# Kernel tuning notes

Hardware: AMD Instinct MI355X
Metric: run time of the kernel (lower is better)

## Reference

```python
import jax, jax.numpy as jnp
import numpy as np

N = 50000
E = 800000
IN_DIM = 128
OUT_DIM = 128


def setup_inputs() -> dict:
    key = jax.random.key(0)
    k1, k2, k3, k4 = jax.random.split(key, 4)
    x = jax.random.normal(k1, (N, IN_DIM), dtype=jnp.float32)
    edge_index = jax.random.randint(k2, (2, E), 0, N, dtype=jnp.int64)
    # Linear(in_dim*2, out_dim) params
    W = jax.random.normal(k3, (2 * IN_DIM, OUT_DIM), dtype=jnp.float32) * (1.0 / np.sqrt(2 * IN_DIM))
    b = jax.random.normal(k4, (OUT_DIM,), dtype=jnp.float32) * 0.01
    return {"x": x, "edge_index": edge_index, "W": W, "b": b}


def reference(x, edge_index, W, b):
    src, dst = edge_index[0], edge_index[1]
    diff = x[src] - x[dst]                              # (E, C)
    # segment-max over destination nodes; empty segments get -inf identity
    seg_max = jax.ops.segment_max(diff, dst, num_segments=N)  # (N, C)
    counts = jax.ops.segment_sum(jnp.ones((E,), dtype=jnp.int32), dst, num_segments=N)
    # original code leaves zeros for nodes with no incoming edges
    max_diff = jnp.where((counts > 0)[:, None], seg_max, jnp.zeros_like(seg_max))
    x_cat = jnp.concatenate([x, max_diff], axis=-1)     # (N, 2C)
    return x_cat @ W + b
```

## Files before the change

### kernel.cpp

```cpp
#include <hip/hip_runtime.h>
#include <math.h>

#define NN 50000
#define NE 800000
#define CD 128
#define LINKB 1600

typedef __attribute__((ext_vector_type(8))) short short8;
typedef __attribute__((ext_vector_type(4))) float f32x4;


__device__ inline unsigned pack2bf(float lo, float hi) {
    unsigned a = __float_as_uint(lo), b = __float_as_uint(hi);
    a = (a + 0x7fffu + ((a >> 16) & 1u)) >> 16;
    b = (b + 0x7fffu + ((b >> 16) & 1u)) & 0xffff0000u;
    return a | b;
}

__device__ inline unsigned short f2bf(float f) {
    unsigned u = __float_as_uint(f);
    return (unsigned short)((u + 0x7fffu + ((u >> 16) & 1u)) >> 16);
}

__device__ inline void fmax8(float* m, uint4 v) {
    m[0] = fmaxf(m[0], __uint_as_float(v.x << 16));
    m[1] = fmaxf(m[1], __uint_as_float(v.x & 0xffff0000u));
    m[2] = fmaxf(m[2], __uint_as_float(v.y << 16));
    m[3] = fmaxf(m[3], __uint_as_float(v.y & 0xffff0000u));
    m[4] = fmaxf(m[4], __uint_as_float(v.z << 16));
    m[5] = fmaxf(m[5], __uint_as_float(v.z & 0xffff0000u));
    m[6] = fmaxf(m[6], __uint_as_float(v.w << 16));
    m[7] = fmaxf(m[7], __uint_as_float(v.w & 0xffff0000u));
}


__global__ __launch_bounds__(256) void prep2_k(const int* __restrict__ ei,
                                               const float* __restrict__ x,
                                               const float* __restrict__ W,
                                               int* __restrict__ head,
                                               int* __restrict__ next,
                                               unsigned* __restrict__ xb,
                                               unsigned short* __restrict__ wt) {
    int b = blockIdx.x;
    int t = threadIdx.x;
    if (b < LINKB) {
        for (int e = b * 256 + t; e < NE; e += LINKB * 256) {
            int d = ei[NE + e];
            int old = atomicExch(&head[d], e);
            next[e] = old;
        }
    } else {
        int tid = (b - LINKB) * 256 + t;
        if (tid < NN * CD / 4) {
            float4 v = ((const float4*)x)[tid];
            uint2 r;
            r.x = pack2bf(v.x, v.y);
            r.y = pack2bf(v.z, v.w);
            ((uint2*)xb)[tid] = r;
        } else {
            int i = tid - NN * CD / 4;
            if (i < 2 * CD * CD) {
                int n = i >> 8, k = i & 255;
                wt[(size_t)n * 256 + k] = f2bf(W[(size_t)k * 128 + n]);
            }
        }
    }
}


__global__ __launch_bounds__(256) void fused_k(const unsigned* __restrict__ xb,
                                               const int* __restrict__ head,
                                               const int* __restrict__ next,
                                               const int* __restrict__ srcp,
                                               const short* __restrict__ wt,
                                               const float* __restrict__ bias,
                                               float* __restrict__ out) {
    __shared__ unsigned short idx[64][68];
    __shared__ int ovf[64];
    __shared__ unsigned short amx[64][136];

    int t = threadIdx.x;
    int nbase = blockIdx.x * 64;

    if (t < 64) {
        int node = nbase + t;
        int e = (node < NN) ? head[node] : -1;
        int cnt = 0;
        while (e >= 0 && cnt < 64) {
            idx[t][cnt] = (unsigned short)srcp[e];
            e = next[e];
            cnt++;
        }
        idx[t][64] = (unsigned short)cnt;
        ovf[t] = e;
    }
    __syncthreads();

    int w = t >> 6, lane = t & 63;
    int q = lane >> 4, c = lane & 15;
#pragma unroll 1
    for (int j = 0; j < 4; j++) {
        int ln = w * 16 + j * 4 + q;
        int node = nbase + ln;
        int cnt = idx[ln][64];
        float m[8];
#pragma unroll
        for (int i = 0; i < 8; i++) m[i] = -INFINITY;

        for (int base = 0; base < cnt; base += 4) {
            uint2 packed = *(const uint2*)&idx[ln][base];
            int s0 = (int)(packed.x & 0xffffu);
            int s1 = (int)(packed.x >> 16);
            int s2 = (int)(packed.y & 0xffffu);
            int s3 = (int)(packed.y >> 16);
            if (base + 0 < cnt) fmax8(m, *(const uint4*)(xb + (size_t)s0 * 64 + c * 4));
            if (base + 1 < cnt) fmax8(m, *(const uint4*)(xb + (size_t)s1 * 64 + c * 4));
            if (base + 2 < cnt) fmax8(m, *(const uint4*)(xb + (size_t)s2 * 64 + c * 4));
            if (base + 3 < cnt) fmax8(m, *(const uint4*)(xb + (size_t)s3 * 64 + c * 4));
        }
        int e = ovf[ln];
        while (e >= 0) {
            int s = srcp[e];
            fmax8(m, *(const uint4*)(xb + (size_t)s * 64 + c * 4));
            e = next[e];
        }
        uint4 r = make_uint4(0u, 0u, 0u, 0u);
        if (cnt > 0) {
            uint4 xd = *(const uint4*)(xb + (size_t)node * 64 + c * 4);
            float d0 = m[0] - __uint_as_float(xd.x << 16);
            float d1 = m[1] - __uint_as_float(xd.x & 0xffff0000u);
            float d2 = m[2] - __uint_as_float(xd.y << 16);
            float d3 = m[3] - __uint_as_float(xd.y & 0xffff0000u);
            float d4 = m[4] - __uint_as_float(xd.z << 16);
            float d5 = m[5] - __uint_as_float(xd.z & 0xffff0000u);
            float d6 = m[6] - __uint_as_float(xd.w << 16);
            float d7 = m[7] - __uint_as_float(xd.w & 0xffff0000u);
            r.x = pack2bf(d0, d1);
            r.y = pack2bf(d2, d3);
            r.z = pack2bf(d4, d5);
            r.w = pack2bf(d6, d7);
        }
        *(uint4*)&amx[ln][c * 8] = r;
    }
    __syncthreads();

    int mm = lane & 15, g = lane >> 4;
    int r0 = nbase + w * 16;
    int row = r0 + mm;
    bool rowok = row < NN;

    f32x4 acc[8];
#pragma unroll
    for (int ct = 0; ct < 8; ct++) {
        float bv = bias[ct * 16 + mm];
        acc[ct] = (f32x4){bv, bv, bv, bv};
    }

    const short* xbs = (const short*)xb;
#pragma unroll
    for (int kc = 0; kc < 8; kc++) {
        int k0 = kc * 32;
        short8 a;
        if (kc < 4) {
            a = (short8){0, 0, 0, 0, 0, 0, 0, 0};
            if (rowok) a = *(const short8*)(xbs + (size_t)row * 128 + k0 + g * 8);
        } else {
            a = *(const short8*)&amx[w * 16 + mm][(k0 - 128) + g * 8];
        }
#pragma unroll
        for (int ct = 0; ct < 8; ct++) {
            short8 b = *(const short8*)(wt + (size_t)(ct * 16 + mm) * 256 + k0 + g * 8);
            acc[ct] = __builtin_amdgcn_mfma_f32_16x16x32_bf16(a, b, acc[ct], 0, 0, 0);
        }
    }

#pragma unroll
    for (int ct = 0; ct < 8; ct++) {
#pragma unroll
        for (int i = 0; i < 4; i++) {
            int rr = r0 + g * 4 + i;
            if (rr < NN) out[(size_t)rr * 128 + ct * 16 + mm] = acc[ct][i];
        }
    }
}


extern "C" void kernel_launch(void* const* d_in, const int* in_sizes, int n_in,
                              void* d_out, int out_size, void* d_ws, size_t ws_size,
                              hipStream_t stream) {
    const float* x = (const float*)d_in[0];
    const int* ei = (const int*)d_in[1];
    const float* W = (const float*)d_in[2];
    const float* bias = (const float*)d_in[3];
    float* out = (float*)d_out;

    int* wsi = (int*)d_ws;
    int* head = wsi;
    int* next = wsi + 50048;
    unsigned* xb  = (unsigned*)(wsi + 850048);
    unsigned short* wt = (unsigned short*)(wsi + 4050048);

    hipMemsetAsync(head, 0xFF, NN * sizeof(int), stream);

    int cast_blocks = (NN * CD / 4 + 2 * CD * CD + 255) / 256;
    prep2_k<<<LINKB + cast_blocks, 256, 0, stream>>>(ei, x, W, head, next, xb, wt);
    fused_k<<<(NN + 63) / 64, 256, 0, stream>>>(xb, head, next, ei, (const short*)wt,
                                                bias, out);
}
```

Measured before the change: 197.4 us.

## Pack src index with next pointer, rebalance prep, use 512-thread fused blocks

Stores each edge's source index together with its linked-list next pointer in one 64-bit word, so the list walk does one dependent load per edge instead of two. The prep kernel now interleaves the linking and x-to-bf16 casting phases across a fixed grid, with odd and even blocks swapping order. The fused kernel doubles its block to 512 threads: each wave gathers for fewer nodes and the GEMM splits output columns across two wave groups. Gathers are unrolled by 8 to keep more loads in flight. The cost is a larger next array and more workspace.

```diff
diff --git a/kernel.cpp b/kernel.cpp
--- a/kernel.cpp
+++ b/kernel.cpp
@@ -4,10 +4,11 @@
 #define NN 50000
 #define NE 800000
 #define CD 128
-#define LINKB 1600
+#define PB 3200
 
 typedef __attribute__((ext_vector_type(8))) short short8;
 typedef __attribute__((ext_vector_type(4))) float f32x4;
+typedef unsigned long long ull;
 
 
 __device__ inline unsigned pack2bf(float lo, float hi) {
@@ -34,48 +35,49 @@
 }
 
 
-__global__ __launch_bounds__(256) void prep2_k(const int* __restrict__ ei,
+__global__ __launch_bounds__(256) void prep3_k(const int* __restrict__ ei,
                                                const float* __restrict__ x,
                                                const float* __restrict__ W,
                                                int* __restrict__ head,
-                                               int* __restrict__ next,
+                                               ull* __restrict__ nxt2,
                                                unsigned* __restrict__ xb,
                                                unsigned short* __restrict__ wt) {
-    int b = blockIdx.x;
-    int t = threadIdx.x;
-    if (b < LINKB) {
-        for (int e = b * 256 + t; e < NE; e += LINKB * 256) {
-            int d = ei[NE + e];
-            int old = atomicExch(&head[d], e);
-            next[e] = old;
-        }
-    } else {
-        int tid = (b - LINKB) * 256 + t;
-        if (tid < NN * CD / 4) {
-            float4 v = ((const float4*)x)[tid];
-            uint2 r;
-            r.x = pack2bf(v.x, v.y);
-            r.y = pack2bf(v.z, v.w);
-            ((uint2*)xb)[tid] = r;
+    int tid0 = blockIdx.x * 256 + threadIdx.x;
+    int phase = blockIdx.x & 1;
+
+    for (int p = 0; p < 2; p++) {
+        if ((p ^ phase) == 0) {
+            for (int e = tid0; e < NE; e += PB * 256) {
+                int d = ei[NE + e];
+                unsigned s = (unsigned)ei[e];
+                int old = atomicExch(&head[d], e);
+                nxt2[e] = ((ull)s << 32) | (unsigned)old;
+            }
         } else {
-            int i = tid - NN * CD / 4;
-            if (i < 2 * CD * CD) {
-                int n = i >> 8, k = i & 255;
-                wt[(size_t)n * 256 + k] = f2bf(W[(size_t)k * 128 + n]);
+            for (int i = tid0; i < NN * CD / 4; i += PB * 256) {
+                float4 v = ((const float4*)x)[i];
+                uint2 r;
+                r.x = pack2bf(v.x, v.y);
+                r.y = pack2bf(v.z, v.w);
+                ((uint2*)xb)[i] = r;
             }
         }
     }
-}
-
-
-__global__ __launch_bounds__(256) void fused_k(const unsigned* __restrict__ xb,
+    for (int i = tid0; i < 2 * CD * CD; i += PB * 256) {
+        int n = i >> 8, k = i & 255;
+        wt[(size_t)n * 256 + k] = f2bf(W[(size_t)k * 128 + n]);
+    }
+}
+
+
+__global__ __launch_bounds__(512) void fused_k(const unsigned* __restrict__ xb,
                                                const int* __restrict__ head,
-                                               const int* __restrict__ next,
-                                               const int* __restrict__ srcp,
+                                               const ull* __restrict__ nxt2,
                                                const short* __restrict__ wt,
                                                const float* __restrict__ bias,
                                                float* __restrict__ out) {
-    __shared__ unsigned short idx[64][68];
+    __shared__ unsigned short idx[64][72];
+    __shared__ unsigned short deg[64];
     __shared__ int ovf[64];
     __shared__ unsigned short amx[64][136];
 
@@ -87,11 +89,12 @@
         int e = (node < NN) ? head[node] : -1;
         int cnt = 0;
         while (e >= 0 && cnt < 64) {
-            idx[t][cnt] = (unsigned short)srcp[e];
-            e = next[e];
+            ull v = nxt2[e];
+            idx[t][cnt] = (unsigned short)(v >> 32);
+            e = (int)(unsigned)(v & 0xffffffffu);
             cnt++;
         }
-        idx[t][64] = (unsigned short)cnt;
+        deg[t] = (unsigned short)cnt;
         ovf[t] = e;
     }
     __syncthreads();
@@ -99,30 +102,46 @@
     int w = t >> 6, lane = t & 63;
     int q = lane >> 4, c = lane & 15;
 #pragma unroll 1
-    for (int j = 0; j < 4; j++) {
-        int ln = w * 16 + j * 4 + q;
+    for (int j = 0; j < 2; j++) {
+        int ln = w * 8 + j * 4 + q;
         int node = nbase + ln;
-        int cnt = idx[ln][64];
+        int cnt = deg[ln];
         float m[8];
 #pragma unroll
         for (int i = 0; i < 8; i++) m[i] = -INFINITY;
 
-        for (int base = 0; base < cnt; base += 4) {
-            uint2 packed = *(const uint2*)&idx[ln][base];
-            int s0 = (int)(packed.x & 0xffffu);
-            int s1 = (int)(packed.x >> 16);
-            int s2 = (int)(packed.y & 0xffffu);
-            int s3 = (int)(packed.y >> 16);
-            if (base + 0 < cnt) fmax8(m, *(const uint4*)(xb + (size_t)s0 * 64 + c * 4));
-            if (base + 1 < cnt) fmax8(m, *(const uint4*)(xb + (size_t)s1 * 64 + c * 4));
-            if (base + 2 < cnt) fmax8(m, *(const uint4*)(xb + (size_t)s2 * 64 + c * 4));
-            if (base + 3 < cnt) fmax8(m, *(const uint4*)(xb + (size_t)s3 * 64 + c * 4));
+        for (int base = 0; base < cnt; base += 8) {
+            uint4 pk = *(const uint4*)&idx[ln][base];
+            int s0 = (int)(pk.x & 0xffffu), s1 = (int)(pk.x >> 16);
+            int s2 = (int)(pk.y & 0xffffu), s3 = (int)(pk.y >> 16);
+            int s4 = (int)(pk.z & 0xffffu), s5 = (int)(pk.z >> 16);
+            int s6 = (int)(pk.w & 0xffffu), s7 = (int)(pk.w >> 16);
+            if (base + 8 <= cnt) {
+                fmax8(m, *(const uint4*)(xb + (size_t)s0 * 64 + c * 4));
+                fmax8(m, *(const uint4*)(xb + (size_t)s1 * 64 + c * 4));
+                fmax8(m, *(const uint4*)(xb + (size_t)s2 * 64 + c * 4));
+                fmax8(m, *(const uint4*)(xb + (size_t)s3 * 64 + c * 4));
+                fmax8(m, *(const uint4*)(xb + (size_t)s4 * 64 + c * 4));
+                fmax8(m, *(const uint4*)(xb + (size_t)s5 * 64 + c * 4));
+                fmax8(m, *(const uint4*)(xb + (size_t)s6 * 64 + c * 4));
+                fmax8(m, *(const uint4*)(xb + (size_t)s7 * 64 + c * 4));
+            } else {
+                if (base + 0 < cnt) fmax8(m, *(const uint4*)(xb + (size_t)s0 * 64 + c * 4));
+                if (base + 1 < cnt) fmax8(m, *(const uint4*)(xb + (size_t)s1 * 64 + c * 4));
+                if (base + 2 < cnt) fmax8(m, *(const uint4*)(xb + (size_t)s2 * 64 + c * 4));
+                if (base + 3 < cnt) fmax8(m, *(const uint4*)(xb + (size_t)s3 * 64 + c * 4));
+                if (base + 4 < cnt) fmax8(m, *(const uint4*)(xb + (size_t)s4 * 64 + c * 4));
+                if (base + 5 < cnt) fmax8(m, *(const uint4*)(xb + (size_t)s5 * 64 + c * 4));
+                if (base + 6 < cnt) fmax8(m, *(const uint4*)(xb + (size_t)s6 * 64 + c * 4));
+                if (base + 7 < cnt) fmax8(m, *(const uint4*)(xb + (size_t)s7 * 64 + c * 4));
+            }
         }
         int e = ovf[ln];
         while (e >= 0) {
-            int s = srcp[e];
+            ull v = nxt2[e];
+            int s = (int)(v >> 32);
             fmax8(m, *(const uint4*)(xb + (size_t)s * 64 + c * 4));
-            e = next[e];
+            e = (int)(unsigned)(v & 0xffffffffu);
         }
         uint4 r = make_uint4(0u, 0u, 0u, 0u);
         if (cnt > 0) {
@@ -145,14 +164,15 @@
     __syncthreads();
 
     int mm = lane & 15, g = lane >> 4;
-    int r0 = nbase + w * 16;
+    int rt = w & 3, ch = w >> 2;
+    int r0 = nbase + rt * 16;
     int row = r0 + mm;
     bool rowok = row < NN;
 
-    f32x4 acc[8];
-#pragma unroll
-    for (int ct = 0; ct < 8; ct++) {
-        float bv = bias[ct * 16 + mm];
+    f32x4 acc[4];
+#pragma unroll
+    for (int ct = 0; ct < 4; ct++) {
+        float bv = bias[ch * 64 + ct * 16 + mm];
         acc[ct] = (f32x4){bv, bv, bv, bv};
     }
 
@@ -165,21 +185,21 @@
             a = (short8){0, 0, 0, 0, 0, 0, 0, 0};
             if (rowok) a = *(const short8*)(xbs + (size_t)row * 128 + k0 + g * 8);
         } else {
-            a = *(const short8*)&amx[w * 16 + mm][(k0 - 128) + g * 8];
-        }
-#pragma unroll
-        for (int ct = 0; ct < 8; ct++) {
-            short8 b = *(const short8*)(wt + (size_t)(ct * 16 + mm) * 256 + k0 + g * 8);
+            a = *(const short8*)&amx[rt * 16 + mm][(k0 - 128) + g * 8];
+        }
+#pragma unroll
+        for (int ct = 0; ct < 4; ct++) {
+            short8 b = *(const short8*)(wt + (size_t)(ch * 64 + ct * 16 + mm) * 256 + k0 + g * 8);
             acc[ct] = __builtin_amdgcn_mfma_f32_16x16x32_bf16(a, b, acc[ct], 0, 0, 0);
         }
     }
 
 #pragma unroll
-    for (int ct = 0; ct < 8; ct++) {
+    for (int ct = 0; ct < 4; ct++) {
 #pragma unroll
         for (int i = 0; i < 4; i++) {
             int rr = r0 + g * 4 + i;
-            if (rr < NN) out[(size_t)rr * 128 + ct * 16 + mm] = acc[ct][i];
+            if (rr < NN) out[(size_t)rr * 128 + ch * 64 + ct * 16 + mm] = acc[ct][i];
         }
     }
 }
@@ -196,14 +216,13 @@
 
     int* wsi = (int*)d_ws;
     int* head = wsi;
-    int* next = wsi + 50048;
-    unsigned* xb  = (unsigned*)(wsi + 850048);
-    unsigned short* wt = (unsigned short*)(wsi + 4050048);
+    ull* nxt2 = (ull*)(wsi + 50048);
+    unsigned* xb  = (unsigned*)(wsi + 1650048);
+    unsigned short* wt = (unsigned short*)(wsi + 4850048);
 
     hipMemsetAsync(head, 0xFF, NN * sizeof(int), stream);
 
-    int cast_blocks = (NN * CD / 4 + 2 * CD * CD + 255) / 256;
-    prep2_k<<<LINKB + cast_blocks, 256, 0, stream>>>(ei, x, W, head, next, xb, wt);
-    fused_k<<<(NN + 63) / 64, 256, 0, stream>>>(xb, head, next, ei, (const short*)wt,
+    prep3_k<<<PB, 256, 0, stream>>>(ei, x, W, head, nxt2, xb, wt);
+    fused_k<<<(NN + 63) / 64, 512, 0, stream>>>(xb, head, nxt2, (const short*)wt,
                                                 bias, out);
 }
```

Result: faster. 186.5 us (-5.5%).
